# Performance work log

Hardware: AMD Instinct MI355X
Metric: run time of the kernel (lower is better)

The kernel has to match this reference:

```python
import jax, jax.numpy as jnp
import numpy as np

B, S, V, D = 64, 256, 50000, 300
NW, CL, CV, CD = 8192, 16, 500, 30
H, T, CH = 128, 17, 30


def setup_inputs() -> dict:
    key = jax.random.key(0)
    ks = jax.random.split(key, 32)
    f32 = jnp.float32
    def rn(k, shape, scale=0.1):
        return jax.random.normal(k, shape, dtype=f32) * scale
    inp = {}
    inp["char_emb"] = rn(ks[0], (CV, CD)).at[0].set(0.0)  # padding_idx=0
    inp["conv_w"] = rn(ks[1], (CH, CD, 3))  # OIH
    inp["conv_b"] = rn(ks[2], (CH,))
    inp["word_emb"] = rn(ks[3], (V, D))
    in0, in1 = D + CH, 2 * H
    inp["w_ih_l0"] = rn(ks[4], (2, 3 * H, in0))  # [dir, 3H, in]
    inp["w_hh_l0"] = rn(ks[5], (2, 3 * H, H))
    inp["b_ih_l0"] = rn(ks[6], (2, 3 * H))
    inp["b_hh_l0"] = rn(ks[7], (2, 3 * H))
    inp["w_ih_l1"] = rn(ks[8], (2, 3 * H, in1))
    inp["w_hh_l1"] = rn(ks[9], (2, 3 * H, H))
    inp["b_ih_l1"] = rn(ks[10], (2, 3 * H))
    inp["b_hh_l1"] = rn(ks[11], (2, 3 * H))
    inp["mlp_w1"] = rn(ks[12], (2 * H, H))
    inp["mlp_b1"] = rn(ks[13], (H,))
    inp["mlp_w2"] = rn(ks[14], (H, T))
    inp["mlp_b2"] = rn(ks[15], (T,))
    inp["crf_start"] = rn(ks[16], (T,))
    inp["crf_end"] = rn(ks[17], (T,))
    inp["crf_trans"] = rn(ks[18], (T, T))
    inp["batched_char_words"] = jax.random.randint(ks[19], (NW, CL), 0, CV)
    inp["batched_char_words_len"] = jax.random.randint(ks[20], (NW,), 1, CL + 1)
    inp["batched_char_word_index"] = jax.random.randint(ks[21], (B, S), 0, NW + 1)
    inp["batched_tokens"] = jax.random.randint(ks[22], (B, S), 0, V)
    inp["batched_tokens_len"] = jax.random.randint(ks[23], (B,), S // 2, S + 1)
    inp["target"] = jax.random.randint(ks[24], (B, S), 0, T)
    return inp


def _gru_dir(x, mask, w_ih, w_hh, b_ih, b_hh, reverse):
    # x: [B,S,I], mask: [B,S] bool. Masked (padded) steps carry hidden state
    # through unchanged, matching pack_padded_sequence semantics.
    xg = jnp.einsum('bsi,gi->sbg', x, w_ih) + b_ih  # [S,B,3H]
    m = mask.T  # [S,B]
    h0 = jnp.zeros((x.shape[0], w_hh.shape[1]), x.dtype)

    def step(h, inp):
        xt, mt = inp
        hg = h @ w_hh.T + b_hh
        xr, xz, xn = jnp.split(xt, 3, axis=-1)
        hr, hz, hn = jnp.split(hg, 3, axis=-1)
        r = jax.nn.sigmoid(xr + hr)
        z = jax.nn.sigmoid(xz + hz)
        n = jnp.tanh(xn + r * hn)
        hnew = (1.0 - z) * n + z * h
        h = jnp.where(mt[:, None], hnew, h)
        return h, h

    _, hs = jax.lax.scan(step, h0, (xg, m), reverse=reverse)
    return hs.transpose(1, 0, 2)  # [B,S,H]


def _bigru_layer(x, mask, w_ih, w_hh, b_ih, b_hh):
    fwd = _gru_dir(x, mask, w_ih[0], w_hh[0], b_ih[0], b_hh[0], False)
    bwd = _gru_dir(x, mask, w_ih[1], w_hh[1], b_ih[1], b_hh[1], True)
    return jnp.concatenate([fwd, bwd], axis=-1)


def _forward(char_emb, conv_w, conv_b, word_emb,
             w_ih_l0, w_hh_l0, b_ih_l0, b_hh_l0,
             w_ih_l1, w_hh_l1, b_ih_l1, b_hh_l1,
             mlp_w1, mlp_b1, mlp_w2, mlp_b2,
             crf_start, crf_end, crf_trans,
             batched_char_words, batched_char_word_index,
             batched_tokens, batched_tokens_len, target):
    # --- char CNN token encoder: conv1d(k=3, SAME) + relu + max-over-time ---
    ct = char_emb[batched_char_words]  # [NW,CL,CD]
    c = jax.lax.conv_general_dilated(ct.transpose(0, 2, 1), conv_w, (1,), 'SAME',
                                     dimension_numbers=('NCH', 'OIH', 'NCH'))
    c = jax.nn.relu(c + conv_b[None, :, None])
    tok_enc = jnp.max(c, axis=-1)  # [NW,CH]
    tok_enc = jnp.concatenate([jnp.zeros((1, tok_enc.shape[1]), tok_enc.dtype), tok_enc], axis=0)
    tok_idx = tok_enc[batched_char_word_index]  # [B,S,CH] (index 0 -> zeros)

    texts = jnp.concatenate([word_emb[batched_tokens], tok_idx], axis=-1)  # [B,S,D+CH]
    seq = batched_tokens.shape[1]
    mask = jnp.arange(seq)[None, :] < batched_tokens_len[:, None]  # [B,S]

    # --- 2-layer BiGRU ---
    h = _bigru_layer(texts, mask, w_ih_l0, w_hh_l0, b_ih_l0, b_hh_l0)
    h = _bigru_layer(h, mask, w_ih_l1, w_hh_l1, b_ih_l1, b_hh_l1)

    # --- MLP head -> emissions [B,S,17] ---
    h = jax.nn.relu(h @ mlp_w1 + mlp_b1)
    emissions = h @ mlp_w2 + mlp_b2

    # --- CRF negative log-likelihood, reduction='token_mean' ---
    maskf = mask.astype(emissions.dtype)
    emit_sc = jnp.take_along_axis(emissions, target[..., None], axis=-1)[..., 0]  # [B,S]
    trans_sc = crf_trans[target[:, :-1], target[:, 1:]]  # [B,S-1]
    score = crf_start[target[:, 0]] + emit_sc[:, 0]
    score = score + jnp.sum((trans_sc + emit_sc[:, 1:]) * maskf[:, 1:], axis=1)
    last_tags = jnp.take_along_axis(target, (batched_tokens_len - 1)[:, None], axis=1)[:, 0]
    score = score + crf_end[last_tags]

    alpha0 = crf_start[None, :] + emissions[:, 0]  # [B,T]
    em_rest = emissions[:, 1:].transpose(1, 0, 2)  # [S-1,B,T]
    m_rest = mask[:, 1:].T  # [S-1,B]

    def crf_step(alpha, inp):
        emit, mt = inp
        new = jax.nn.logsumexp(alpha[:, :, None] + crf_trans[None], axis=1) + emit
        return jnp.where(mt[:, None], new, alpha), None

    alpha, _ = jax.lax.scan(crf_step, alpha0, (em_rest, m_rest))
    log_z = jax.nn.logsumexp(alpha + crf_end[None, :], axis=1)
    llh = score - log_z
    return -(jnp.sum(llh) / jnp.sum(maskf))


def reference(char_emb, conv_w, conv_b, word_emb,
              w_ih_l0, w_hh_l0, b_ih_l0, b_hh_l0,
              w_ih_l1, w_hh_l1, b_ih_l1, b_hh_l1,
              mlp_w1, mlp_b1, mlp_w2, mlp_b2,
              crf_start, crf_end, crf_trans,
              batched_char_words, batched_char_words_len,
              batched_char_word_index, batched_tokens, batched_tokens_len, target):
    return _forward(char_emb, conv_w, conv_b, word_emb,
                    w_ih_l0, w_hh_l0, b_ih_l0, b_hh_l0,
                    w_ih_l1, w_hh_l1, b_ih_l1, b_hh_l1,
                    mlp_w1, mlp_b1, mlp_w2, mlp_b2,
                    crf_start, crf_end, crf_trans,
                    batched_char_words, batched_char_word_index,
                    batched_tokens, batched_tokens_len, target)
```

## Files before the change

kernel.cpp:

```cpp
#include <hip/hip_runtime.h>
#include <cstddef>

#define BATCH 64
#define SEQ   256
#define VOCAB 50000
#define DIM   300
#define NW    8192
#define CLEN  16
#define CDIM  30
#define CHC   30
#define HID   128
#define NT    17
#define IN0   (DIM + CHC)
#define IN0P  336
#define IN1   (2 * HID)
#define NPOS  (BATCH * SEQ)

constexpr size_t SZ_XG    = 2ull * BATCH * SEQ * 384;
constexpr size_t SZ_TEXTS = (size_t)NPOS * IN0P;
constexpr size_t SZ_H1    = (size_t)NPOS * 256;
constexpr size_t SZ_TOK   = 245792;
constexpr size_t SZ_EMIS  = (size_t)NPOS * NT;
constexpr size_t SZ_WPAD  = 768ull * IN0P;
constexpr size_t OFF_XG    = 0;
constexpr size_t OFF_TEXTS = OFF_XG + SZ_XG;
constexpr size_t OFF_H1    = OFF_TEXTS + SZ_TEXTS;
constexpr size_t OFF_TOK   = OFF_H1 + SZ_H1;
constexpr size_t OFF_EMIS  = OFF_TOK + SZ_TOK;
constexpr size_t OFF_WPAD  = OFF_EMIS + SZ_EMIS;
constexpr size_t OFF_LLH   = OFF_WPAD + SZ_WPAD;

__device__ __forceinline__ float sigm(float x) {
    return 1.f / (1.f + __expf(-x));
}
__device__ __forceinline__ float tanh_fast(float x) {
    x = fminf(fmaxf(x, -15.f), 15.f);
    float e = __expf(-2.f * x);
    return (1.f - e) / (1.f + e);
}
__device__ __forceinline__ float dot4(float4 a, float4 b) {
    return a.x * b.x + a.y * b.y + a.z * b.z + a.w * b.w;
}
__device__ __forceinline__ float quad_sum(float x) {
    int y = __builtin_amdgcn_update_dpp(0, __float_as_int(x), 0xB1, 0xF, 0xF, false);
    x += __int_as_float(y);
    y = __builtin_amdgcn_update_dpp(0, __float_as_int(x), 0x4E, 0xF, 0xF, false);
    x += __int_as_float(y);
    return x;
}
__device__ __forceinline__ float xor4_add(float x) {
    int y = __builtin_amdgcn_ds_swizzle(__float_as_int(x), 0x101F);
    return x + __int_as_float(y);
}

__global__ __launch_bounds__(256) void char_conv_k(
    const float* __restrict__ char_emb,
    const float* __restrict__ conv_w,
    const float* __restrict__ conv_b,
    const int*   __restrict__ words,
    float* __restrict__ tok_enc)
{
    __shared__ __align__(16) float cs[8][CLEN][CDIM];
    __shared__ float wsm[CHC * CDIM * 3];
    __shared__ float bs[CHC];
    int n0 = blockIdx.x * 8;
    int tid = threadIdx.x;
    for (int e = tid; e < CHC * CDIM * 3; e += 256) wsm[e] = conv_w[e];
    if (tid < CHC) bs[tid] = conv_b[tid];
    for (int e = tid; e < 8 * CLEN * CDIM; e += 256) {
        int wi = e / (CLEN * CDIM);
        int rem = e - wi * (CLEN * CDIM);
        int l = rem / CDIM;
        int i = rem - l * CDIM;
        int ci = words[(n0 + wi) * CLEN + l];
        cs[wi][l][i] = char_emb[ci * CDIM + i];
    }
    __syncthreads();
    int wi = tid >> 5;
    int o = tid & 31;
    if (o < CHC) {
        float best = -1e30f;
        for (int l = 0; l < CLEN; l++) {
            float s = 0.f;
            #pragma unroll
            for (int k = 0; k < 3; k++) {
                int ll = l + k - 1;
                if (ll >= 0 && ll < CLEN) {
                    #pragma unroll
                    for (int i = 0; i < CDIM; i++)
                        s += cs[wi][ll][i] * wsm[(o * CDIM + i) * 3 + k];
                }
            }
            best = fmaxf(best, s);
        }
        tok_enc[(size_t)(n0 + wi + 1) * CDIM + o] = fmaxf(best + bs[o], 0.f);
    }
}

__global__ __launch_bounds__(128) void build_texts_k(
    const float* __restrict__ word_emb,
    const float* __restrict__ tok_enc,
    const int*   __restrict__ tokens,
    const int*   __restrict__ widx,
    float* __restrict__ texts)
{
    int p = blockIdx.x;
    int tok = tokens[p];
    int ci = widx[p];
    float* o = texts + (size_t)p * IN0P;
    const float* wr = word_emb + (size_t)tok * DIM;
    const float* tr = tok_enc + (size_t)ci * CDIM;
    for (int c = threadIdx.x; c < IN0P; c += 128)
        o[c] = (c < DIM) ? wr[c] : (c < IN0 ? tr[c - DIM] : 0.f);
}

__global__ __launch_bounds__(64) void pad_w_k(
    const float* __restrict__ w, float* __restrict__ wp)
{
    int r = blockIdx.x;
    for (int c = threadIdx.x; c < IN0P; c += 64)
        wp[(size_t)r * IN0P + c] = (c < IN0) ? w[(size_t)r * IN0 + c] : 0.f;
}

#define GBM 128
#define GBN 128
#define GBK 16
__global__ __launch_bounds__(256, 3) void gemm_xg_k(
    const float* __restrict__ A,
    const float* __restrict__ W,
    const float* __restrict__ bias,
    float* __restrict__ out,
    int K)
{
    __shared__ __align__(16) float As[2][GBK][GBM];
    __shared__ __align__(16) float Ws[2][GBK][GBN];
    int tid = threadIdx.x;
    int B = blockIdx.y * gridDim.x + blockIdx.x;
    int X = B & 7;
    int idx = B >> 3;
    int mt = X * 16 + idx / 6;
    int nt = idx - (idx / 6) * 6;
    int n0 = nt * GBN;
    int m0 = mt * GBM;
    int lrow = tid >> 1;
    int lk = (tid & 1) * 8;
    int ty = tid >> 4;
    int tx = tid & 15;

    const float* ap = A + (size_t)(m0 + lrow) * K + lk;
    const float* wpt = W + (size_t)(n0 + lrow) * K + lk;

    float acc[8][8];
    #pragma unroll
    for (int i = 0; i < 8; i++)
        #pragma unroll
        for (int j = 0; j < 8; j++) acc[i][j] = 0.f;

    float4 a0 = *(const float4*)(ap);
    float4 a1 = *(const float4*)(ap + 4);
    float4 w0 = *(const float4*)(wpt);
    float4 w1 = *(const float4*)(wpt + 4);
    {
        float* as = &As[0][lk][lrow];
        as[0*GBM] = a0.x; as[1*GBM] = a0.y; as[2*GBM] = a0.z; as[3*GBM] = a0.w;
        as[4*GBM] = a1.x; as[5*GBM] = a1.y; as[6*GBM] = a1.z; as[7*GBM] = a1.w;
        float* wsp = &Ws[0][lk][lrow];
        wsp[0*GBN] = w0.x; wsp[1*GBN] = w0.y; wsp[2*GBN] = w0.z; wsp[3*GBN] = w0.w;
        wsp[4*GBN] = w1.x; wsp[5*GBN] = w1.y; wsp[6*GBN] = w1.z; wsp[7*GBN] = w1.w;
    }
    __syncthreads();

    int nk = K / GBK;
    int cur = 0;
    for (int it = 1; it < nk; it++) {
        const float* apn = ap + it * GBK;
        const float* wpn = wpt + it * GBK;
        a0 = *(const float4*)(apn);
        a1 = *(const float4*)(apn + 4);
        w0 = *(const float4*)(wpn);
        w1 = *(const float4*)(wpn + 4);
        #pragma unroll
        for (int k = 0; k < GBK; k++) {
            float4 va0 = *(const float4*)&As[cur][k][ty * 8];
            float4 va1 = *(const float4*)&As[cur][k][ty * 8 + 4];
            float4 vb0 = *(const float4*)&Ws[cur][k][tx * 4];
            float4 vb1 = *(const float4*)&Ws[cur][k][64 + tx * 4];
            float av[8] = {va0.x, va0.y, va0.z, va0.w, va1.x, va1.y, va1.z, va1.w};
            float bv[8] = {vb0.x, vb0.y, vb0.z, vb0.w, vb1.x, vb1.y, vb1.z, vb1.w};
            #pragma unroll
            for (int i = 0; i < 8; i++)
                #pragma unroll
                for (int j = 0; j < 8; j++)
                    acc[i][j] += av[i] * bv[j];
        }
        int nb = cur ^ 1;
        {
            float* as = &As[nb][lk][lrow];
            as[0*GBM] = a0.x; as[1*GBM] = a0.y; as[2*GBM] = a0.z; as[3*GBM] = a0.w;
            as[4*GBM] = a1.x; as[5*GBM] = a1.y; as[6*GBM] = a1.z; as[7*GBM] = a1.w;
            float* wsp = &Ws[nb][lk][lrow];
            wsp[0*GBN] = w0.x; wsp[1*GBN] = w0.y; wsp[2*GBN] = w0.z; wsp[3*GBN] = w0.w;
            wsp[4*GBN] = w1.x; wsp[5*GBN] = w1.y; wsp[6*GBN] = w1.z; wsp[7*GBN] = w1.w;
        }
        __syncthreads();
        cur = nb;
    }
    #pragma unroll
    for (int k = 0; k < GBK; k++) {
        float4 va0 = *(const float4*)&As[cur][k][ty * 8];
        float4 va1 = *(const float4*)&As[cur][k][ty * 8 + 4];
        float4 vb0 = *(const float4*)&Ws[cur][k][tx * 4];
        float4 vb1 = *(const float4*)&Ws[cur][k][64 + tx * 4];
        float av[8] = {va0.x, va0.y, va0.z, va0.w, va1.x, va1.y, va1.z, va1.w};
        float bv[8] = {vb0.x, vb0.y, vb0.z, vb0.w, vb1.x, vb1.y, vb1.z, vb1.w};
        #pragma unroll
        for (int i = 0; i < 8; i++)
            #pragma unroll
            for (int j = 0; j < 8; j++)
                acc[i][j] += av[i] * bv[j];
    }

    int c0 = n0 + tx * 4;
    int d = (c0 >= 384) ? 1 : 0;
    int g0 = c0 - d * 384;
    float4 bb0 = *(const float4*)(bias + c0);
    float4 bb1 = *(const float4*)(bias + c0 + 64);
    int mbase = m0 + ty * 8;
    #pragma unroll
    for (int i = 0; i < 8; i++) {
        int m = mbase + i;
        int b = m >> 8;
        int t = m & 255;
        float* op = out + (((size_t)(d * BATCH + b) * SEQ + t) * 384);
        float4 r0, r1;
        r0.x = acc[i][0] + bb0.x; r0.y = acc[i][1] + bb0.y;
        r0.z = acc[i][2] + bb0.z; r0.w = acc[i][3] + bb0.w;
        r1.x = acc[i][4] + bb1.x; r1.y = acc[i][5] + bb1.y;
        r1.z = acc[i][6] + bb1.z; r1.w = acc[i][7] + bb1.w;
        *(float4*)(op + g0) = r0;
        *(float4*)(op + g0 + 64) = r1;
    }
}

__global__ __launch_bounds__(512, 2) void gru_rec_k(
    const float* __restrict__ xg,
    const float* __restrict__ w_hh,
    const float* __restrict__ b_hh,
    const int*   __restrict__ lens,
    float* __restrict__ out)
{
    int d = blockIdx.x & 1;
    int b = blockIdx.x >> 1;
    int i = threadIdx.x;
    int c = i & 7;
    int e2 = i >> 3;
    int sel = c & 1;
    int eSel = e2 + 64 * sel;
    __shared__ __align__(16) float hS[2][HID];

    int mj[4];
    #pragma unroll
    for (int j = 0; j < 4; j++) mj[j] = (j + (c >> 1)) & 3;

    const float* wb = w_hh + (size_t)d * 384 * HID;
    float4 wR0[4], wZ0[4], wN0[4], wR1[4], wZ1[4], wN1[4];
    #pragma unroll
    for (int j = 0; j < 4; j++) {
        int off = 16 * c + 4 * mj[j];
        wR0[j] = *(const float4*)(wb + (size_t)(e2)       * HID + off);
        wZ0[j] = *(const float4*)(wb + (size_t)(128 + e2) * HID + off);
        wN0[j] = *(const float4*)(wb + (size_t)(256 + e2) * HID + off);
        wR1[j] = *(const float4*)(wb + (size_t)(64 + e2)  * HID + off);
        wZ1[j] = *(const float4*)(wb + (size_t)(192 + e2) * HID + off);
        wN1[j] = *(const float4*)(wb + (size_t)(320 + e2) * HID + off);
    }
    float bhR = b_hh[d * 384 + eSel];
    float bhZ = b_hh[d * 384 + 128 + eSel];
    float bhN = b_hh[d * 384 + 256 + eSel];
    int len = lens[b];

    if (i < HID) hS[0][i] = 0.f;
    float hold = 0.f;
    __syncthreads();

    const float* xgb = xg + ((size_t)(d * BATCH + b)) * SEQ * 384;
    float* outb = out + (size_t)b * SEQ * 256 + d * HID;

    int t0 = d ? (SEQ - 1) : 0;
    float xvR = xgb[(size_t)t0 * 384 + eSel];
    float xvZ = xgb[(size_t)t0 * 384 + 128 + eSel];
    float xvN = xgb[(size_t)t0 * 384 + 256 + eSel];
    int tPrev = t0;

    int idxA = c * 4 + mj[0];
    int idxB = c * 4 + mj[1];
    int idxC = c * 4 + mj[2];
    int idxD = c * 4 + mj[3];

    for (int s = 0; s < SEQ; s++) {
        int t = d ? (SEQ - 1 - s) : s;
        if (s && c < 2) outb[(size_t)tPrev * 256 + eSel] = hold;
        int sn = (s + 1 < SEQ) ? (s + 1) : s;
        int tn = d ? (SEQ - 1 - sn) : sn;
        float nxvR = xgb[(size_t)tn * 384 + eSel];
        float nxvZ = xgb[(size_t)tn * 384 + 128 + eSel];
        float nxvN = xgb[(size_t)tn * 384 + 256 + eSel];

        const float4* hb = (const float4*)hS[s & 1];
        float4 hv0 = hb[idxA];
        float4 hv1 = hb[idxB];
        float4 hv2 = hb[idxC];
        float4 hv3 = hb[idxD];

        float sR0 = dot4(wR0[0], hv0) + dot4(wR0[1], hv1) + dot4(wR0[2], hv2) + dot4(wR0[3], hv3);
        float sZ0 = dot4(wZ0[0], hv0) + dot4(wZ0[1], hv1) + dot4(wZ0[2], hv2) + dot4(wZ0[3], hv3);
        float sN0 = dot4(wN0[0], hv0) + dot4(wN0[1], hv1) + dot4(wN0[2], hv2) + dot4(wN0[3], hv3);
        float sR1 = dot4(wR1[0], hv0) + dot4(wR1[1], hv1) + dot4(wR1[2], hv2) + dot4(wR1[3], hv3);
        float sZ1 = dot4(wZ1[0], hv0) + dot4(wZ1[1], hv1) + dot4(wZ1[2], hv2) + dot4(wZ1[3], hv3);
        float sN1 = dot4(wN1[0], hv0) + dot4(wN1[1], hv1) + dot4(wN1[2], hv2) + dot4(wN1[3], hv3);

        sR0 = quad_sum(sR0); sZ0 = quad_sum(sZ0); sN0 = quad_sum(sN0);
        sR1 = quad_sum(sR1); sZ1 = quad_sum(sZ1); sN1 = quad_sum(sN1);
        float sR = xor4_add(sel ? sR1 : sR0);
        float sZ = xor4_add(sel ? sZ1 : sZ0);
        float sN = xor4_add(sel ? sN1 : sN0);

        float r = sigm(xvR + sR + bhR);
        float z = sigm(xvZ + sZ + bhZ);
        float n = tanh_fast(xvN + r * (sN + bhN));
        float hnew = (1.f - z) * n + z * hold;
        hold = (t < len) ? hnew : hold;
        if (c < 2) hS[(s & 1) ^ 1][eSel] = hold;
        tPrev = t;
        xvR = nxvR; xvZ = nxvZ; xvN = nxvN;
        __syncthreads();
    }
    if (c < 2) outb[(size_t)tPrev * 256 + eSel] = hold;
}

__global__ __launch_bounds__(128) void mlp_emis_k(
    const float* __restrict__ h1,
    const float* __restrict__ w1,
    const float* __restrict__ b1,
    const float* __restrict__ w2,
    const float* __restrict__ b2,
    float* __restrict__ emis)
{
    __shared__ __align__(16) float hrow[8 * 256];
    __shared__ float hid[8][HID];
    int p0 = blockIdx.x * 8;
    int tid = threadIdx.x;
    for (int e = tid; e < 8 * 256; e += 128)
        hrow[e] = h1[(size_t)p0 * 256 + e];
    __syncthreads();
    float acc[8];
    float bb = b1[tid];
    #pragma unroll
    for (int i = 0; i < 8; i++) acc[i] = bb;
    for (int k = 0; k < 256; k++) {
        float wv = w1[k * HID + tid];
        #pragma unroll
        for (int i = 0; i < 8; i++) acc[i] += hrow[i * 256 + k] * wv;
    }
    #pragma unroll
    for (int i = 0; i < 8; i++) hid[i][tid] = fmaxf(acc[i], 0.f);
    __syncthreads();
    for (int idx = tid; idx < 8 * NT; idx += 128) {
        int pos = idx / NT;
        int tg = idx - pos * NT;
        float a = b2[tg];
        for (int k = 0; k < HID; k++) a += hid[pos][k] * w2[k * NT + tg];
        emis[(size_t)(p0 + pos) * NT + tg] = a;
    }
}

__global__ __launch_bounds__(64) void crf_k(
    const float* __restrict__ emis,
    const float* __restrict__ start,
    const float* __restrict__ endv,
    const float* __restrict__ trans,
    const int*   __restrict__ target,
    const int*   __restrict__ lens,
    float* __restrict__ llh)
{
    int b = blockIdx.x;
    int tid = threadIdx.x;
    __shared__ float tr[NT * NT];
    __shared__ float aSh[NT];
    __shared__ float scoreSh;
    for (int e = tid; e < NT * NT; e += 64) tr[e] = trans[e];
    __syncthreads();
    int len = lens[b];
    const int* tgt = target + b * SEQ;
    const float* eb = emis + (size_t)b * SEQ * NT;

    float part = 0.f;
    for (int t = 1 + tid; t < SEQ; t += 64) {
        if (t < len) {
            int tp = tgt[t - 1], tc = tgt[t];
            part += tr[tp * NT + tc] + eb[(size_t)t * NT + tc];
        }
    }
    #pragma unroll
    for (int off = 32; off > 0; off >>= 1)
        part += __shfl_down(part, off, 64);
    if (tid == 0) {
        int t0 = tgt[0];
        scoreSh = part + start[t0] + eb[t0] + endv[tgt[len - 1]];
    }

    float a = (tid < NT) ? (start[tid] + eb[tid]) : 0.f;
    for (int t = 1; t < SEQ; t++) {
        if (tid < NT) aSh[tid] = a;
        __syncthreads();
        if (t < len && tid < NT) {
            float m = -1e30f;
            #pragma unroll
            for (int i = 0; i < NT; i++)
                m = fmaxf(m, aSh[i] + tr[i * NT + tid]);
            float ssum = 0.f;
            #pragma unroll
            for (int i = 0; i < NT; i++)
                ssum += __expf(aSh[i] + tr[i * NT + tid] - m);
            a = m + __logf(ssum) + eb[(size_t)t * NT + tid];
        }
        __syncthreads();
    }
    float v = (tid < NT) ? (a + endv[tid]) : -1e30f;
    float m = v;
    #pragma unroll
    for (int off = 32; off > 0; off >>= 1)
        m = fmaxf(m, __shfl_down(m, off, 64));
    m = __shfl(m, 0, 64);
    float e = (tid < NT) ? __expf(v - m) : 0.f;
    #pragma unroll
    for (int off = 32; off > 0; off >>= 1)
        e += __shfl_down(e, off, 64);
    if (tid == 0) {
        float logz = m + __logf(e);
        llh[b] = scoreSh - logz;
    }
}

__global__ __launch_bounds__(64) void finalize_k(
    const float* __restrict__ llh,
    const int*   __restrict__ lens,
    float* __restrict__ out)
{
    int tid = threadIdx.x;
    float s = llh[tid];
    float lf = (float)lens[tid];
    #pragma unroll
    for (int off = 32; off > 0; off >>= 1) {
        s += __shfl_down(s, off, 64);
        lf += __shfl_down(lf, off, 64);
    }
    if (tid == 0) out[0] = -(s / lf);
}

extern "C" void kernel_launch(void* const* d_in, const int* in_sizes, int n_in,
                              void* d_out, int out_size, void* d_ws, size_t ws_size,
                              hipStream_t stream) {
    const float* char_emb = (const float*)d_in[0];
    const float* conv_w   = (const float*)d_in[1];
    const float* conv_b   = (const float*)d_in[2];
    const float* word_emb = (const float*)d_in[3];
    const float* w_ih_l0  = (const float*)d_in[4];
    const float* w_hh_l0  = (const float*)d_in[5];
    const float* b_ih_l0  = (const float*)d_in[6];
    const float* b_hh_l0  = (const float*)d_in[7];
    const float* w_ih_l1  = (const float*)d_in[8];
    const float* w_hh_l1  = (const float*)d_in[9];
    const float* b_ih_l1  = (const float*)d_in[10];
    const float* b_hh_l1  = (const float*)d_in[11];
    const float* mlp_w1   = (const float*)d_in[12];
    const float* mlp_b1   = (const float*)d_in[13];
    const float* mlp_w2   = (const float*)d_in[14];
    const float* mlp_b2   = (const float*)d_in[15];
    const float* crf_start= (const float*)d_in[16];
    const float* crf_end  = (const float*)d_in[17];
    const float* crf_trans= (const float*)d_in[18];
    const int* bcw   = (const int*)d_in[19];
    const int* bcwi  = (const int*)d_in[21];
    const int* btok  = (const int*)d_in[22];
    const int* blen  = (const int*)d_in[23];
    const int* target= (const int*)d_in[24];

    float* ws    = (float*)d_ws;
    float* xg    = ws + OFF_XG;
    float* texts = ws + OFF_TEXTS;
    float* h0    = texts;
    float* h1    = ws + OFF_H1;
    float* tok   = ws + OFF_TOK;
    float* emis  = ws + OFF_EMIS;
    float* wpad  = ws + OFF_WPAD;
    float* llh   = ws + OFF_LLH;

    hipMemsetAsync(tok, 0, CDIM * sizeof(float), stream);
    pad_w_k<<<768, 64, 0, stream>>>(w_ih_l0, wpad);
    char_conv_k<<<NW / 8, 256, 0, stream>>>(char_emb, conv_w, conv_b, bcw, tok);
    build_texts_k<<<NPOS, 128, 0, stream>>>(word_emb, tok, btok, bcwi, texts);
    gemm_xg_k<<<dim3(768 / GBN, NPOS / GBM), 256, 0, stream>>>(texts, wpad, b_ih_l0, xg, IN0P);
    gru_rec_k<<<2 * BATCH, 512, 0, stream>>>(xg, w_hh_l0, b_hh_l0, blen, h0);
    gemm_xg_k<<<dim3(768 / GBN, NPOS / GBM), 256, 0, stream>>>(h0, w_ih_l1, b_ih_l1, xg, IN1);
    gru_rec_k<<<2 * BATCH, 512, 0, stream>>>(xg, w_hh_l1, b_hh_l1, blen, h1);
    mlp_emis_k<<<NPOS / 8, 128, 0, stream>>>(h1, mlp_w1, mlp_b1, mlp_w2, mlp_b2, emis);
    crf_k<<<BATCH, 64, 0, stream>>>(emis, crf_start, crf_end, crf_trans, target, blen, llh);
    finalize_k<<<1, 64, 0, stream>>>(llh, blen, (float*)d_out);
}
```

Measured before the change: 946.4 us.

## Stream GEMM weights from global into registers; use DPP mirror in GRU reduction

```diff
diff --git a/kernel.cpp b/kernel.cpp
--- a/kernel.cpp
+++ b/kernel.cpp
@@ -41,6 +41,9 @@
 __device__ __forceinline__ float dot4(float4 a, float4 b) {
     return a.x * b.x + a.y * b.y + a.z * b.z + a.w * b.w;
 }
+__device__ __forceinline__ float getc(float4 v, int c) {
+    return c == 0 ? v.x : c == 1 ? v.y : c == 2 ? v.z : v.w;
+}
 __device__ __forceinline__ float quad_sum(float x) {
     int y = __builtin_amdgcn_update_dpp(0, __float_as_int(x), 0xB1, 0xF, 0xF, false);
     x += __int_as_float(y);
@@ -48,8 +51,8 @@
     x += __int_as_float(y);
     return x;
 }
-__device__ __forceinline__ float xor4_add(float x) {
-    int y = __builtin_amdgcn_ds_swizzle(__float_as_int(x), 0x101F);
+__device__ __forceinline__ float mirror8_add(float x) {
+    int y = __builtin_amdgcn_update_dpp(0, __float_as_int(x), 0x141, 0xF, 0xF, false);
     return x + __int_as_float(y);
 }
 
@@ -133,7 +136,6 @@
     int K)
 {
     __shared__ __align__(16) float As[2][GBK][GBM];
-    __shared__ __align__(16) float Ws[2][GBK][GBN];
     int tid = threadIdx.x;
     int B = blockIdx.y * gridDim.x + blockIdx.x;
     int X = B & 7;
@@ -148,7 +150,10 @@
     int tx = tid & 15;
 
     const float* ap = A + (size_t)(m0 + lrow) * K + lk;
-    const float* wpt = W + (size_t)(n0 + lrow) * K + lk;
+    const float* wb2 = W + (size_t)64 * K;
+    int rowK[4];
+    #pragma unroll
+    for (int j = 0; j < 4; j++) rowK[j] = (n0 + tx * 4 + j) * K;
 
     float acc[8][8];
     #pragma unroll
@@ -156,68 +161,64 @@
         #pragma unroll
         for (int j = 0; j < 8; j++) acc[i][j] = 0.f;
 
-    float4 a0 = *(const float4*)(ap);
-    float4 a1 = *(const float4*)(ap + 4);
-    float4 w0 = *(const float4*)(wpt);
-    float4 w1 = *(const float4*)(wpt + 4);
     {
+        float4 a0 = *(const float4*)(ap);
+        float4 a1 = *(const float4*)(ap + 4);
         float* as = &As[0][lk][lrow];
         as[0*GBM] = a0.x; as[1*GBM] = a0.y; as[2*GBM] = a0.z; as[3*GBM] = a0.w;
         as[4*GBM] = a1.x; as[5*GBM] = a1.y; as[6*GBM] = a1.z; as[7*GBM] = a1.w;
-        float* wsp = &Ws[0][lk][lrow];
-        wsp[0*GBN] = w0.x; wsp[1*GBN] = w0.y; wsp[2*GBN] = w0.z; wsp[3*GBN] = w0.w;
-        wsp[4*GBN] = w1.x; wsp[5*GBN] = w1.y; wsp[6*GBN] = w1.z; wsp[7*GBN] = w1.w;
-    }
+    }
+    float4 wc[8], wn[8];
+    #pragma unroll
+    for (int r = 0; r < 8; r++)
+        wc[r] = *(const float4*)((r < 4 ? W : wb2) + rowK[r & 3]);
     __syncthreads();
 
     int nk = K / GBK;
     int cur = 0;
-    for (int it = 1; it < nk; it++) {
-        const float* apn = ap + it * GBK;
-        const float* wpn = wpt + it * GBK;
-        a0 = *(const float4*)(apn);
-        a1 = *(const float4*)(apn + 4);
-        w0 = *(const float4*)(wpn);
-        w1 = *(const float4*)(wpn + 4);
+
+    auto k4body = [&](int kl, int knext, float4* WU, float4* WL) {
         #pragma unroll
-        for (int k = 0; k < GBK; k++) {
-            float4 va0 = *(const float4*)&As[cur][k][ty * 8];
-            float4 va1 = *(const float4*)&As[cur][k][ty * 8 + 4];
-            float4 vb0 = *(const float4*)&Ws[cur][k][tx * 4];
-            float4 vb1 = *(const float4*)&Ws[cur][k][64 + tx * 4];
+        for (int r = 0; r < 8; r++)
+            WL[r] = *(const float4*)((r < 4 ? W : wb2) + rowK[r & 3] + knext);
+        #pragma unroll
+        for (int kk = 0; kk < 4; kk++) {
+            const float* asp = &As[cur][kl + kk][ty * 8];
+            float4 va0 = *(const float4*)(asp);
+            float4 va1 = *(const float4*)(asp + 4);
             float av[8] = {va0.x, va0.y, va0.z, va0.w, va1.x, va1.y, va1.z, va1.w};
-            float bv[8] = {vb0.x, vb0.y, vb0.z, vb0.w, vb1.x, vb1.y, vb1.z, vb1.w};
             #pragma unroll
             for (int i = 0; i < 8; i++)
                 #pragma unroll
-                for (int j = 0; j < 8; j++)
-                    acc[i][j] += av[i] * bv[j];
+                for (int r = 0; r < 8; r++)
+                    acc[i][r] += av[i] * getc(WU[r], kk);
         }
+    };
+
+    for (int it = 0; it < nk - 1; it++) {
+        const float* apn = ap + (it + 1) * GBK;
+        float4 na0 = *(const float4*)(apn);
+        float4 na1 = *(const float4*)(apn + 4);
+        int kb = it * GBK;
+        k4body(0,  kb + 4,  wc, wn);
+        k4body(4,  kb + 8,  wn, wc);
+        k4body(8,  kb + 12, wc, wn);
+        k4body(12, kb + 16, wn, wc);
         int nb = cur ^ 1;
         {
             float* as = &As[nb][lk][lrow];
-            as[0*GBM] = a0.x; as[1*GBM] = a0.y; as[2*GBM] = a0.z; as[3*GBM] = a0.w;
-            as[4*GBM] = a1.x; as[5*GBM] = a1.y; as[6*GBM] = a1.z; as[7*GBM] = a1.w;
-            float* wsp = &Ws[nb][lk][lrow];
-            wsp[0*GBN] = w0.x; wsp[1*GBN] = w0.y; wsp[2*GBN] = w0.z; wsp[3*GBN] = w0.w;
-            wsp[4*GBN] = w1.x; wsp[5*GBN] = w1.y; wsp[6*GBN] = w1.z; wsp[7*GBN] = w1.w;
+            as[0*GBM] = na0.x; as[1*GBM] = na0.y; as[2*GBM] = na0.z; as[3*GBM] = na0.w;
+            as[4*GBM] = na1.x; as[5*GBM] = na1.y; as[6*GBM] = na1.z; as[7*GBM] = na1.w;
         }
         __syncthreads();
         cur = nb;
     }
-    #pragma unroll
-    for (int k = 0; k < GBK; k++) {
-        float4 va0 = *(const float4*)&As[cur][k][ty * 8];
-        float4 va1 = *(const float4*)&As[cur][k][ty * 8 + 4];
-        float4 vb0 = *(const float4*)&Ws[cur][k][tx * 4];
-        float4 vb1 = *(const float4*)&Ws[cur][k][64 + tx * 4];
-        float av[8] = {va0.x, va0.y, va0.z, va0.w, va1.x, va1.y, va1.z, va1.w};
-        float bv[8] = {vb0.x, vb0.y, vb0.z, vb0.w, vb1.x, vb1.y, vb1.z, vb1.w};
-        #pragma unroll
-        for (int i = 0; i < 8; i++)
-            #pragma unroll
-            for (int j = 0; j < 8; j++)
-                acc[i][j] += av[i] * bv[j];
+    {
+        int kb = (nk - 1) * GBK;
+        k4body(0,  kb + 4,  wc, wn);
+        k4body(4,  kb + 8,  wn, wc);
+        k4body(8,  kb + 12, wc, wn);
+        k4body(12, 0,       wn, wc);
     }
 
     int c0 = n0 + tx * 4;
@@ -254,7 +255,7 @@
     int i = threadIdx.x;
     int c = i & 7;
     int e2 = i >> 3;
-    int sel = c & 1;
+    int sel = (c ^ (c >> 1)) & 1;
     int eSel = e2 + 64 * sel;
     __shared__ __align__(16) float hS[2][HID];
 
@@ -321,9 +322,9 @@
 
         sR0 = quad_sum(sR0); sZ0 = quad_sum(sZ0); sN0 = quad_sum(sN0);
         sR1 = quad_sum(sR1); sZ1 = quad_sum(sZ1); sN1 = quad_sum(sN1);
-        float sR = xor4_add(sel ? sR1 : sR0);
-        float sZ = xor4_add(sel ? sZ1 : sZ0);
-        float sN = xor4_add(sel ? sN1 : sN0);
+        float sR = mirror8_add(sel ? sR1 : sR0);
+        float sZ = mirror8_add(sel ? sZ1 : sZ0);
+        float sN = mirror8_add(sel ? sN1 : sN0);
 
         float r = sigm(xvR + sR + bhR);
         float z = sigm(xvZ + sZ + bhZ);
```

Measured after the change: 1.245 ms. +31.6%, slower.
